# Kernel optimization log

Measured on AMD Instinct MI355X. Metric: run time of the kernel, lower is better.

## Reference

```python
import jax, jax.numpy as jnp
import numpy as np

N_EMBD = 1024
N_HEADS = 16
HEAD_DIM = N_EMBD // N_HEADS


def setup_inputs() -> dict:
    key = jax.random.key(0)
    ks = jax.random.split(key, 6)
    s = 1.0 / np.sqrt(N_EMBD)
    x = jax.random.normal(ks[0], (2, 2048, N_EMBD), dtype=jnp.float32)
    # torch Linear weights are [out, in]; y = x @ W.T
    Wk = jax.random.uniform(ks[1], (N_EMBD, N_EMBD), jnp.float32, -s, s)
    Wq = jax.random.uniform(ks[2], (N_EMBD, N_EMBD), jnp.float32, -s, s)
    Wv = jax.random.uniform(ks[3], (N_EMBD, N_EMBD), jnp.float32, -s, s)
    Wp = jax.random.uniform(ks[4], (N_EMBD, N_EMBD), jnp.float32, -s, s)
    bp = jax.random.uniform(ks[5], (N_EMBD,), jnp.float32, -s, s)
    return {"x": x, "Wq": Wq, "Wk": Wk, "Wv": Wv, "Wp": Wp, "bp": bp}


def reference(x, Wq, Wk, Wv, Wp, bp):
    B, T, C = x.shape
    H, D = N_HEADS, HEAD_DIM
    # projections (torch Linear: x @ W.T), reshape to [B, H, T, D]
    q = (x @ Wq.T).reshape(B, T, H, D).transpose(0, 2, 1, 3)
    k = (x @ Wk.T).reshape(B, T, H, D).transpose(0, 2, 1, 3)
    v = (x @ Wv.T).reshape(B, T, H, D).transpose(0, 2, 1, 3)
    # scaled causal attention, full [B,H,T,T] scores (faithful to original)
    att = jnp.einsum('bhqd,bhkd->bhqk', q, k) * (D ** -0.5)
    causal = jnp.tril(jnp.ones((T, T), dtype=bool))
    att = jnp.where(causal[None, None], att, -jnp.inf)
    att = jax.nn.softmax(att, axis=-1)
    out = jnp.einsum('bhqk,bhkd->bhqd', att, v)
    out = out.transpose(0, 2, 1, 3).reshape(B, T, C)
    return out @ Wp.T + bp
```

## Files before the change

kernel.cpp:

```cpp
#include <hip/hip_runtime.h>

typedef __bf16 bf16;
typedef __bf16 bf16x8 __attribute__((ext_vector_type(8)));
typedef float f32x4 __attribute__((ext_vector_type(4)));

#define DEV __device__ __forceinline__
#define NEG_BIG (-1.0e30f)


DEV bf16x8 load8(const bf16* p) { bf16x8 v; __builtin_memcpy(&v, p, 16); return v; }
DEV void store8(bf16* p, bf16x8 v) { __builtin_memcpy(p, &v, 16); }

DEV int sniff_bf16(const unsigned short* __restrict__ xr) {
  const int lane = threadIdx.x & 63;
  const unsigned short w = xr[lane * 2];
  const int e = (w >> 7) & 0xFF;
  const bool sane = ((w & 0x7FFF) == 0) || (e >= 97 && e <= 157);
  return __popcll(__ballot(sane)) >= 48;
}

DEV size_t frag_off(int row, int k) {
  const int rt = row >> 7, ks = k >> 6;
  const int chunk = (((row >> 4) & 7) * 2 + ((k >> 5) & 1)) * 64 + ((k >> 3) & 3) * 16 + (row & 15);
  return ((((size_t)rt * 16 + (size_t)ks) * 1024 + (size_t)chunk) << 3) | (size_t)(k & 7);
}

struct ConvArgs {
  const void* src[6];
  bf16* dst[6];
  int n[6];
};

__global__ __launch_bounds__(256) void convert_kernel(ConvArgs a) {
  const int isbf = sniff_bf16((const unsigned short*)a.src[0]);
  const int t = blockIdx.y;
  const int n = a.n[t];
  bf16* d = a.dst[t];
  const int stride = gridDim.x * 256 * 8;
  const bool frag = (t < 5);
  for (int i = (blockIdx.x * 256 + threadIdx.x) * 8; i < n; i += stride) {
    bf16x8 v;
    if (isbf) {
      v = load8((const bf16*)a.src[t] + i);
    } else {
      float tmp[8];
      __builtin_memcpy(tmp, (const float*)a.src[t] + i, 32);
#pragma unroll
      for (int j = 0; j < 8; ++j) v[j] = (bf16)tmp[j];
    }
    if (frag) store8(d + frag_off(i >> 10, i & 1023), v);
    else      store8(d + i, v);
  }
}

DEV void gemm_reg_128(const bf16* __restrict__ A, const bf16* __restrict__ W,
                      int mblk, int nblk, f32x4 (&acc)[4][4]) {
  const int lane = threadIdx.x & 63, wid = threadIdx.x >> 6;
  const int wm = (wid >> 1) << 6, wn = (wid & 1) << 6;
  const int lr = lane & 15, lg = lane >> 4;
  const int arow = mblk * 128 + wm + lr;
  const int brow = nblk * 128 + wn + lr;

  const f32x4 zero = {0.f, 0.f, 0.f, 0.f};
#pragma unroll
  for (int i = 0; i < 4; ++i)
#pragma unroll
    for (int j = 0; j < 4; ++j) acc[i][j] = zero;

  for (int ks = 0; ks < 16; ++ks) {
    bf16x8 af[2][4], bf[2][4];
#pragma unroll
    for (int kh = 0; kh < 2; ++kh) {
      const int k = ks * 64 + kh * 32 + lg * 8;
#pragma unroll
      for (int i = 0; i < 4; ++i) af[kh][i] = load8(A + frag_off(arow + i * 16, k));
#pragma unroll
      for (int j = 0; j < 4; ++j) bf[kh][j] = load8(W + frag_off(brow + j * 16, k));
    }
#pragma unroll
    for (int kh = 0; kh < 2; ++kh)
#pragma unroll
      for (int i = 0; i < 4; ++i)
#pragma unroll
        for (int j = 0; j < 4; ++j)
          acc[i][j] = __builtin_amdgcn_mfma_f32_16x16x32_bf16(af[kh][i], bf[kh][j], acc[i][j], 0, 0, 0);
  }
}

DEV size_t frag_idx(int row, int col) {
  return ((size_t)(((col >> 5) * 4 + ((row >> 4) & 3)) * 64 + ((col >> 3) & 3) * 16 + (row & 15)) << 3)
         | (size_t)(col & 7);
}

__global__ __launch_bounds__(256, 3) void qkv_proj_kernel(
    const bf16* __restrict__ x, const bf16* __restrict__ Wq,
    const bf16* __restrict__ Wk, const bf16* __restrict__ Wv,
    bf16* __restrict__ q_ws, bf16* __restrict__ k_ws, bf16* __restrict__ vt_ws) {
  const int L = blockIdx.x;
  const int xcd = L & 7;
  const int idx = L >> 3;
  const int mblk = (xcd & 3) * 8 + (idx & 7);
  const int nm = (xcd >> 2) * 12 + (idx >> 3);
  const int nblk = nm & 7;
  const int mode = nm >> 3;
  const bf16* W = (mode == 0) ? Wq : (mode == 1) ? Wk : Wv;
  f32x4 acc[4][4];
  gemm_reg_128(x, W, mblk, nblk, acc);

  const int lane = threadIdx.x & 63, wid = threadIdx.x >> 6;
  const int wm = (wid >> 1) << 6, wn = (wid & 1) << 6;
  const int lr = lane & 15, lg = lane >> 4;
  const int m0 = mblk << 7, n0 = nblk << 7;
  bf16* out = (mode == 0) ? q_ws : (mode == 1) ? k_ws : vt_ws;
#pragma unroll
  for (int i = 0; i < 4; ++i) {
#pragma unroll
    for (int r = 0; r < 4; ++r) {
      const int m = m0 + wm + i * 16 + lg * 4 + r;
      const int b = m >> 11, t = m & 2047;
#pragma unroll
      for (int j = 0; j < 4; ++j) {
        const int n = n0 + wn + j * 16 + lr;
        const int h = n >> 6, d = n & 63;
        const float v = acc[i][j][r];
        const size_t base = ((size_t)(b * 16 + h) << 17) + ((size_t)(t >> 6) << 12);
        const size_t idx2 = base + ((mode < 2) ? frag_idx(t & 63, d) : frag_idx(d, t & 63));
        out[idx2] = (bf16)v;
      }
    }
  }
}

__global__ __launch_bounds__(256, 2) void attn_kernel(
    const bf16* __restrict__ q_ws, const bf16* __restrict__ k_ws,
    const bf16* __restrict__ vt_ws, bf16* __restrict__ a_ws) {
  const int L = blockIdx.x;
  const int xcd = L & 7;
  const int bh = xcd * 4 + ((L >> 3) & 3);
  const int pr = L >> 5;
  const int tid = threadIdx.x;
  const int lane = tid & 63, w = tid >> 6;
  const int lr = lane & 15, lg = lane >> 4;
  const int fo = lg * 16 + lr;

  __shared__ alignas(16) bf16 Ps[4][16 * 72];
  bf16* ps = &Ps[w][0];

  const size_t hb = (size_t)bh << 17;
  const int b = bh >> 4, h = bh & 15;
  const f32x4 zero = {0.f, 0.f, 0.f, 0.f};

  for (int ph = 0; ph < 2; ++ph) {
    const int qt = ph ? (31 - pr) : pr;
    const size_t qtb = hb + ((size_t)qt << 12);

    bf16x8 aq[2];
#pragma unroll
    for (int c2 = 0; c2 < 2; ++c2)
      aq[c2] = load8(q_ws + qtb + (size_t)(((c2 * 4 + w) * 64 + fo) << 3));

    f32x4 o_acc[4];
#pragma unroll
    for (int j = 0; j < 4; ++j) o_acc[j] = zero;
    float lsum[4] = {0.f, 0.f, 0.f, 0.f};

    auto load_k = [&](bf16x8 (&bk)[4][2], int kt) {
      const size_t ktb = hb + ((size_t)kt << 12);
#pragma unroll
      for (int j = 0; j < 4; ++j)
#pragma unroll
        for (int c2 = 0; c2 < 2; ++c2)
          bk[j][c2] = load8(k_ws + ktb + (size_t)(((c2 * 4 + j) * 64 + fo) << 3));
    };

    auto step = [&](const bf16x8 (&bk)[4][2], int kt, bool diag) {
      const size_t ktb = hb + ((size_t)kt << 12);
      bf16x8 bv[4][2];
#pragma unroll
      for (int j = 0; j < 4; ++j)
#pragma unroll
        for (int c2 = 0; c2 < 2; ++c2)
          bv[j][c2] = load8(vt_ws + ktb + (size_t)(((c2 * 4 + j) * 64 + fo) << 3));

      f32x4 s[4];
#pragma unroll
      for (int j = 0; j < 4; ++j) {
        s[j] = __builtin_amdgcn_mfma_f32_16x16x32_bf16(aq[0], bk[j][0], zero, 0, 0, 0);
        s[j] = __builtin_amdgcn_mfma_f32_16x16x32_bf16(aq[1], bk[j][1], s[j], 0, 0, 0);
      }
      float p[4][4];
#pragma unroll
      for (int j = 0; j < 4; ++j) {
#pragma unroll
        for (int r = 0; r < 4; ++r) {
          float v = s[j][r] * 0.125f;
          if (diag && (j * 16 + lr) > (w * 16 + lg * 4 + r)) v = NEG_BIG;
          p[j][r] = __expf(v);
        }
      }
#pragma unroll
      for (int r = 0; r < 4; ++r)
        lsum[r] += (p[0][r] + p[1][r]) + (p[2][r] + p[3][r]);
#pragma unroll
      for (int j = 0; j < 4; ++j)
#pragma unroll
        for (int r = 0; r < 4; ++r)
          ps[(lg * 4 + r) * 72 + j * 16 + lr] = (bf16)p[j][r];
#pragma unroll
      for (int c2 = 0; c2 < 2; ++c2) {
        const bf16x8 ap = load8(ps + lr * 72 + c2 * 32 + lg * 8);
#pragma unroll
        for (int j = 0; j < 4; ++j)
          o_acc[j] = __builtin_amdgcn_mfma_f32_16x16x32_bf16(ap, bv[j][c2], o_acc[j], 0, 0, 0);
      }
    };

    bf16x8 bkA[4][2], bkB[4][2];
    const int n = qt;
    load_k(bkA, qt);
    if (n > 0) load_k(bkB, 0);
    step(bkA, qt, true);
    int kt = 0;
    while (kt + 1 < n) {
      load_k(bkA, kt + 1);
      step(bkB, kt, false);
      if (kt + 2 < n) load_k(bkB, kt + 2);
      step(bkA, kt + 1, false);
      kt += 2;
    }
    if (kt < n) step(bkB, kt, false);

    float l_i[4];
#pragma unroll
    for (int r = 0; r < 4; ++r) {
      float v = lsum[r];
#pragma unroll
      for (int off = 1; off < 16; off <<= 1) v += __shfl_xor(v, off, 64);
      l_i[r] = v;
    }

#pragma unroll
    for (int r = 0; r < 4; ++r) {
      const int mrow = b * 2048 + qt * 64 + w * 16 + lg * 4 + r;
      const float inv = 1.f / l_i[r];
#pragma unroll
      for (int j = 0; j < 4; ++j) {
        const int col = h * 64 + j * 16 + lr;
        a_ws[frag_off(mrow, col)] = (bf16)(o_acc[j][r] * inv);
      }
    }
  }
}

__global__ __launch_bounds__(256, 3) void out_proj_kernel(
    const bf16* __restrict__ A, const bf16* __restrict__ Wp,
    const bf16* __restrict__ bp, void* __restrict__ out,
    const unsigned short* __restrict__ xraw) {
  const int L = blockIdx.x;
  const int xcd = L & 7;
  const int i2 = L >> 3;
  const int mblk = xcd * 4 + (i2 & 3);
  const int nblk = i2 >> 2;
  f32x4 acc[4][4];
  gemm_reg_128(A, Wp, mblk, nblk, acc);

  const int lane = threadIdx.x & 63, wid = threadIdx.x >> 6;
  const int wm = (wid >> 1) << 6, wn = (wid & 1) << 6;
  const int lr = lane & 15, lg = lane >> 4;
  const int m0 = mblk << 7, n0 = nblk << 7;
  const int isbf = sniff_bf16(xraw);
#pragma unroll
  for (int i = 0; i < 4; ++i) {
#pragma unroll
    for (int r = 0; r < 4; ++r) {
      const int m = m0 + wm + i * 16 + lg * 4 + r;
#pragma unroll
      for (int j = 0; j < 4; ++j) {
        const int n = n0 + wn + j * 16 + lr;
        const float v = acc[i][j][r] + (float)bp[n];
        const size_t idx = ((size_t)m << 10) | (size_t)n;
        if (isbf) ((bf16*)out)[idx] = (bf16)v;
        else      ((float*)out)[idx] = v;
      }
    }
  }
}

extern "C" void kernel_launch(void* const* d_in, const int* in_sizes, int n_in,
                              void* d_out, int out_size, void* d_ws, size_t ws_size,
                              hipStream_t stream) {
  (void)in_sizes; (void)n_in; (void)out_size;
  if (ws_size < (50u << 20)) return;

  char* ws = (char*)d_ws;
  bf16* q_ws  = (bf16*)(ws);
  bf16* k_ws  = (bf16*)(ws + (8u << 20));
  bf16* vt_ws = (bf16*)(ws + (16u << 20));
  bf16* a_ws  = (bf16*)(ws + (24u << 20));
  bf16* xc    = (bf16*)(ws + (32u << 20));
  bf16* Wqc   = (bf16*)(ws + (40u << 20));
  bf16* Wkc   = (bf16*)(ws + (42u << 20));
  bf16* Wvc   = (bf16*)(ws + (44u << 20));
  bf16* Wpc   = (bf16*)(ws + (46u << 20));
  bf16* bpc   = (bf16*)(ws + (48u << 20));

  ConvArgs ca;
  ca.src[0] = d_in[0]; ca.dst[0] = xc;  ca.n[0] = 4096 * 1024;
  ca.src[1] = d_in[1]; ca.dst[1] = Wqc; ca.n[1] = 1024 * 1024;
  ca.src[2] = d_in[2]; ca.dst[2] = Wkc; ca.n[2] = 1024 * 1024;
  ca.src[3] = d_in[3]; ca.dst[3] = Wvc; ca.n[3] = 1024 * 1024;
  ca.src[4] = d_in[4]; ca.dst[4] = Wpc; ca.n[4] = 1024 * 1024;
  ca.src[5] = d_in[5]; ca.dst[5] = bpc; ca.n[5] = 1024;
  convert_kernel<<<dim3(512, 6), 256, 0, stream>>>(ca);

  qkv_proj_kernel<<<768, 256, 0, stream>>>(xc, Wqc, Wkc, Wvc, q_ws, k_ws, vt_ws);
  attn_kernel<<<512, 256, 0, stream>>>(q_ws, k_ws, vt_ws, a_ws);
  out_proj_kernel<<<256, 256, 0, stream>>>(a_ws, Wpc, bpc, d_out,
                                           (const unsigned short*)d_in[0]);
}
```

Before: 196.6 us.

## Tile convert through LDS, fold softmax scale into Q, restructure attention waves

The convert kernel now processes one 128x64 tile per block and stages it in shared memory, so the fragment-layout scatter becomes coalesced 16-byte writes instead of strided frag_off stores. The 1/sqrt(D) scale moves into the Q projection epilogue, which removes a multiply per score inside attention. Attention blocks drop to two waves, and each wave now owns 32 query rows (two 16-row groups) that share every K/V fragment load, with finer-grained causal balancing across 32-row slabs. In exchange the register footprint per wave grows and there are fewer waves per block, which may reduce latency hiding.

```diff
diff --git a/kernel.cpp b/kernel.cpp
--- a/kernel.cpp
+++ b/kernel.cpp
@@ -28,28 +28,50 @@
 struct ConvArgs {
   const void* src[6];
   bf16* dst[6];
-  int n[6];
 };
+
+DEV bf16x8 cvt_load(const void* s, size_t e, int isbf) {
+  bf16x8 v;
+  if (isbf) v = load8((const bf16*)s + e);
+  else {
+    float tmp[8];
+    __builtin_memcpy(tmp, (const float*)s + e, 32);
+#pragma unroll
+    for (int j = 0; j < 8; ++j) v[j] = (bf16)tmp[j];
+  }
+  return v;
+}
 
 __global__ __launch_bounds__(256) void convert_kernel(ConvArgs a) {
   const int isbf = sniff_bf16((const unsigned short*)a.src[0]);
-  const int t = blockIdx.y;
-  const int n = a.n[t];
-  bf16* d = a.dst[t];
-  const int stride = gridDim.x * 256 * 8;
-  const bool frag = (t < 5);
-  for (int i = (blockIdx.x * 256 + threadIdx.x) * 8; i < n; i += stride) {
-    bf16x8 v;
-    if (isbf) {
-      v = load8((const bf16*)a.src[t] + i);
-    } else {
-      float tmp[8];
-      __builtin_memcpy(tmp, (const float*)a.src[t] + i, 32);
-#pragma unroll
-      for (int j = 0; j < 8; ++j) v[j] = (bf16)tmp[j];
-    }
-    if (frag) store8(d + frag_off(i >> 10, i & 1023), v);
-    else      store8(d + i, v);
+  const int L = blockIdx.x;
+  const int t = threadIdx.x;
+  if (L == 1024) {
+    if (t < 128) store8(a.dst[5] + t * 8, cvt_load(a.src[5], (size_t)t * 8, isbf));
+    return;
+  }
+  int sel, tile;
+  if (L < 512) { sel = 0; tile = L; }
+  else         { sel = 1 + ((L - 512) >> 7); tile = (L - 512) & 127; }
+  const int rt = tile >> 4, ks = tile & 15;
+  const void* s = a.src[sel];
+  bf16* d = a.dst[sel];
+
+  __shared__ alignas(16) bf16 lds[128 * 9 * 8];
+#pragma unroll
+  for (int q = 0; q < 4; ++q) {
+    const int lin = q * 256 + t;
+    const int row = lin >> 3, k8 = lin & 7;
+    const size_t se = (((size_t)(rt * 128 + row)) << 10) + (size_t)(ks * 64 + k8 * 8);
+    store8(lds + (row * 9 + k8) * 8, cvt_load(s, se, isbf));
+  }
+  __syncthreads();
+#pragma unroll
+  for (int q = 0; q < 4; ++q) {
+    const int c = q * 256 + t;
+    const int row = ((c >> 7) & 7) * 16 + (c & 15);
+    const int k8 = ((c >> 6) & 1) * 4 + ((c >> 4) & 3);
+    store8(d + ((((size_t)tile << 10) + (size_t)c) << 3), load8(lds + (row * 9 + k8) * 8));
   }
 }
 
@@ -111,6 +133,7 @@
   const int wm = (wid >> 1) << 6, wn = (wid & 1) << 6;
   const int lr = lane & 15, lg = lane >> 4;
   const int m0 = mblk << 7, n0 = nblk << 7;
+  const float vscale = (mode == 0) ? 0.125f : 1.0f;
   bf16* out = (mode == 0) ? q_ws : (mode == 1) ? k_ws : vt_ws;
 #pragma unroll
   for (int i = 0; i < 4; ++i) {
@@ -122,7 +145,7 @@
       for (int j = 0; j < 4; ++j) {
         const int n = n0 + wn + j * 16 + lr;
         const int h = n >> 6, d = n & 63;
-        const float v = acc[i][j][r];
+        const float v = acc[i][j][r] * vscale;
         const size_t base = ((size_t)(b * 16 + h) << 17) + ((size_t)(t >> 6) << 12);
         const size_t idx2 = base + ((mode < 2) ? frag_idx(t & 63, d) : frag_idx(d, t & 63));
         out[idx2] = (bf16)v;
@@ -131,19 +154,19 @@
   }
 }
 
-__global__ __launch_bounds__(256, 2) void attn_kernel(
+__global__ __launch_bounds__(128, 1) void attn_kernel(
     const bf16* __restrict__ q_ws, const bf16* __restrict__ k_ws,
     const bf16* __restrict__ vt_ws, bf16* __restrict__ a_ws) {
   const int L = blockIdx.x;
   const int xcd = L & 7;
   const int bh = xcd * 4 + ((L >> 3) & 3);
-  const int pr = L >> 5;
+  const int p = L >> 5;
   const int tid = threadIdx.x;
   const int lane = tid & 63, w = tid >> 6;
   const int lr = lane & 15, lg = lane >> 4;
   const int fo = lg * 16 + lr;
 
-  __shared__ alignas(16) bf16 Ps[4][16 * 72];
+  __shared__ alignas(16) bf16 Ps[2][32 * 72];
   bf16* ps = &Ps[w][0];
 
   const size_t hb = (size_t)bh << 17;
@@ -151,18 +174,25 @@
   const f32x4 zero = {0.f, 0.f, 0.f, 0.f};
 
   for (int ph = 0; ph < 2; ++ph) {
-    const int qt = ph ? (31 - pr) : pr;
-    const size_t qtb = hb + ((size_t)qt << 12);
-
-    bf16x8 aq[2];
-#pragma unroll
-    for (int c2 = 0; c2 < 2; ++c2)
-      aq[c2] = load8(q_ws + qtb + (size_t)(((c2 * 4 + w) * 64 + fo) << 3));
-
-    f32x4 o_acc[4];
-#pragma unroll
-    for (int j = 0; j < 4; ++j) o_acc[j] = zero;
-    float lsum[4] = {0.f, 0.f, 0.f, 0.f};
+    const int s = ph ? (63 - (p * 2 + w)) : (p * 2 + w);
+    const int kmax = s >> 1;
+    const size_t qtb = hb + ((size_t)(s >> 1) << 12);
+
+    bf16x8 aq[2][2];
+#pragma unroll
+    for (int g = 0; g < 2; ++g) {
+      const int rg = (s & 1) * 2 + g;
+#pragma unroll
+      for (int c2 = 0; c2 < 2; ++c2)
+        aq[g][c2] = load8(q_ws + qtb + (size_t)(((c2 * 4 + rg) * 64 + fo) << 3));
+    }
+
+    f32x4 o_acc[2][4];
+#pragma unroll
+    for (int g = 0; g < 2; ++g)
+#pragma unroll
+      for (int j = 0; j < 4; ++j) o_acc[g][j] = zero;
+    float lsum[2][4] = {{0.f, 0.f, 0.f, 0.f}, {0.f, 0.f, 0.f, 0.f}};
 
     auto load_k = [&](bf16x8 (&bk)[4][2], int kt) {
       const size_t ktb = hb + ((size_t)kt << 12);
@@ -182,71 +212,81 @@
         for (int c2 = 0; c2 < 2; ++c2)
           bv[j][c2] = load8(vt_ws + ktb + (size_t)(((c2 * 4 + j) * 64 + fo) << 3));
 
-      f32x4 s[4];
-#pragma unroll
-      for (int j = 0; j < 4; ++j) {
-        s[j] = __builtin_amdgcn_mfma_f32_16x16x32_bf16(aq[0], bk[j][0], zero, 0, 0, 0);
-        s[j] = __builtin_amdgcn_mfma_f32_16x16x32_bf16(aq[1], bk[j][1], s[j], 0, 0, 0);
-      }
-      float p[4][4];
-#pragma unroll
-      for (int j = 0; j < 4; ++j) {
-#pragma unroll
-        for (int r = 0; r < 4; ++r) {
-          float v = s[j][r] * 0.125f;
-          if (diag && (j * 16 + lr) > (w * 16 + lg * 4 + r)) v = NEG_BIG;
-          p[j][r] = __expf(v);
+      f32x4 sc[2][4];
+#pragma unroll
+      for (int g = 0; g < 2; ++g)
+#pragma unroll
+        for (int j = 0; j < 4; ++j) {
+          sc[g][j] = __builtin_amdgcn_mfma_f32_16x16x32_bf16(aq[g][0], bk[j][0], zero, 0, 0, 0);
+          sc[g][j] = __builtin_amdgcn_mfma_f32_16x16x32_bf16(aq[g][1], bk[j][1], sc[g][j], 0, 0, 0);
         }
-      }
-#pragma unroll
-      for (int r = 0; r < 4; ++r)
-        lsum[r] += (p[0][r] + p[1][r]) + (p[2][r] + p[3][r]);
-#pragma unroll
-      for (int j = 0; j < 4; ++j)
+      float pp[2][4][4];
+#pragma unroll
+      for (int g = 0; g < 2; ++g) {
+#pragma unroll
+        for (int j = 0; j < 4; ++j) {
+#pragma unroll
+          for (int r = 0; r < 4; ++r) {
+            float v = sc[g][j][r];
+            if (diag) {
+              const int trow = s * 32 + g * 16 + lg * 4 + r;
+              const int tcol = kt * 64 + j * 16 + lr;
+              if (tcol > trow) v = NEG_BIG;
+            }
+            pp[g][j][r] = __expf(v);
+          }
+        }
 #pragma unroll
         for (int r = 0; r < 4; ++r)
-          ps[(lg * 4 + r) * 72 + j * 16 + lr] = (bf16)p[j][r];
+          lsum[g][r] += (pp[g][0][r] + pp[g][1][r]) + (pp[g][2][r] + pp[g][3][r]);
+      }
+#pragma unroll
+      for (int g = 0; g < 2; ++g)
+#pragma unroll
+        for (int j = 0; j < 4; ++j)
+#pragma unroll
+          for (int r = 0; r < 4; ++r)
+            ps[(g * 16 + lg * 4 + r) * 72 + j * 16 + lr] = (bf16)pp[g][j][r];
 #pragma unroll
       for (int c2 = 0; c2 < 2; ++c2) {
-        const bf16x8 ap = load8(ps + lr * 72 + c2 * 32 + lg * 8);
-#pragma unroll
-        for (int j = 0; j < 4; ++j)
-          o_acc[j] = __builtin_amdgcn_mfma_f32_16x16x32_bf16(ap, bv[j][c2], o_acc[j], 0, 0, 0);
+#pragma unroll
+        for (int g = 0; g < 2; ++g) {
+          const bf16x8 ap = load8(ps + (g * 16 + lr) * 72 + c2 * 32 + lg * 8);
+#pragma unroll
+          for (int j = 0; j < 4; ++j)
+            o_acc[g][j] = __builtin_amdgcn_mfma_f32_16x16x32_bf16(ap, bv[j][c2], o_acc[g][j], 0, 0, 0);
+        }
       }
     };
 
     bf16x8 bkA[4][2], bkB[4][2];
-    const int n = qt;
-    load_k(bkA, qt);
-    if (n > 0) load_k(bkB, 0);
-    step(bkA, qt, true);
+    load_k(bkA, 0);
     int kt = 0;
-    while (kt + 1 < n) {
-      load_k(bkA, kt + 1);
-      step(bkB, kt, false);
-      if (kt + 2 < n) load_k(bkB, kt + 2);
-      step(bkA, kt + 1, false);
-      kt += 2;
-    }
-    if (kt < n) step(bkB, kt, false);
-
-    float l_i[4];
-#pragma unroll
-    for (int r = 0; r < 4; ++r) {
-      float v = lsum[r];
-#pragma unroll
-      for (int off = 1; off < 16; off <<= 1) v += __shfl_xor(v, off, 64);
-      l_i[r] = v;
-    }
-
-#pragma unroll
-    for (int r = 0; r < 4; ++r) {
-      const int mrow = b * 2048 + qt * 64 + w * 16 + lg * 4 + r;
-      const float inv = 1.f / l_i[r];
-#pragma unroll
-      for (int j = 0; j < 4; ++j) {
-        const int col = h * 64 + j * 16 + lr;
-        a_ws[frag_off(mrow, col)] = (bf16)(o_acc[j][r] * inv);
+    while (true) {
+      if (kt < kmax) load_k(bkB, kt + 1);
+      step(bkA, kt, kt == kmax);
+      if (kt >= kmax) break;
+      ++kt;
+      if (kt < kmax) load_k(bkA, kt + 1);
+      step(bkB, kt, kt == kmax);
+      if (kt >= kmax) break;
+      ++kt;
+    }
+
+#pragma unroll
+    for (int g = 0; g < 2; ++g) {
+#pragma unroll
+      for (int r = 0; r < 4; ++r) {
+        float v = lsum[g][r];
+#pragma unroll
+        for (int off = 1; off < 16; off <<= 1) v += __shfl_xor(v, off, 64);
+        const float inv = 1.f / v;
+        const int mrow = b * 2048 + s * 32 + g * 16 + lg * 4 + r;
+#pragma unroll
+        for (int j = 0; j < 4; ++j) {
+          const int col = h * 64 + j * 16 + lr;
+          a_ws[frag_off(mrow, col)] = (bf16)(o_acc[g][j][r] * inv);
+        }
       }
     }
   }
@@ -305,16 +345,16 @@
   bf16* bpc   = (bf16*)(ws + (48u << 20));
 
   ConvArgs ca;
-  ca.src[0] = d_in[0]; ca.dst[0] = xc;  ca.n[0] = 4096 * 1024;
-  ca.src[1] = d_in[1]; ca.dst[1] = Wqc; ca.n[1] = 1024 * 1024;
-  ca.src[2] = d_in[2]; ca.dst[2] = Wkc; ca.n[2] = 1024 * 1024;
-  ca.src[3] = d_in[3]; ca.dst[3] = Wvc; ca.n[3] = 1024 * 1024;
-  ca.src[4] = d_in[4]; ca.dst[4] = Wpc; ca.n[4] = 1024 * 1024;
-  ca.src[5] = d_in[5]; ca.dst[5] = bpc; ca.n[5] = 1024;
-  convert_kernel<<<dim3(512, 6), 256, 0, stream>>>(ca);
+  ca.src[0] = d_in[0]; ca.dst[0] = xc;
+  ca.src[1] = d_in[1]; ca.dst[1] = Wqc;
+  ca.src[2] = d_in[2]; ca.dst[2] = Wkc;
+  ca.src[3] = d_in[3]; ca.dst[3] = Wvc;
+  ca.src[4] = d_in[4]; ca.dst[4] = Wpc;
+  ca.src[5] = d_in[5]; ca.dst[5] = bpc;
+  convert_kernel<<<1025, 256, 0, stream>>>(ca);
 
   qkv_proj_kernel<<<768, 256, 0, stream>>>(xc, Wqc, Wkc, Wvc, q_ws, k_ws, vt_ws);
-  attn_kernel<<<512, 256, 0, stream>>>(q_ws, k_ws, vt_ws, a_ws);
+  attn_kernel<<<512, 128, 0, stream>>>(q_ws, k_ws, vt_ws, a_ws);
   out_proj_kernel<<<256, 256, 0, stream>>>(a_ws, Wpc, bpc, d_out,
                                            (const unsigned short*)d_in[0]);
 }
```

New measurement: 209.0 us. 1.06x slower.
